# Kernel optimization log

Measured on AMD Instinct MI355X. Metric: run time of the kernel, lower is better.

## Reference

```python
import jax, jax.numpy as jnp
import numpy as np

K = 16          # num clusters
DZ = 64         # dim_zt == dim_zi (required by decoder matmul)
DT = 1024       # treatment feature dim (dim_t)
NT = 2048       # number of treatments == dim_x (columns of input_ins)
NI = 4096       # number of instances
MU_P_WT = 5.0
COS_EPS = 1e-6


def setup_inputs() -> dict:
    key = jax.random.key(0)
    ks = jax.random.split(key, 12)
    s = 0.02
    return {
        "input_ins": jax.random.uniform(ks[0], (NI, NT), dtype=jnp.float32),
        "input_treat": jax.random.normal(ks[1], (NT, DT), dtype=jnp.float32),
        # nn.Linear params (torch layout: W [out, in], y = x @ W.T + b)
        "W_mu_zt": jax.random.normal(ks[2], (DZ, DT)) * s,
        "b_mu_zt": jnp.zeros((DZ,), jnp.float32),
        "W_lv_zt": jax.random.normal(ks[3], (DZ, DT)) * s,
        "b_lv_zt": jnp.zeros((DZ,), jnp.float32),
        "W_arec": jax.random.normal(ks[4], (DT, DZ)) * s,
        "b_arec": jnp.zeros((DT,), jnp.float32),
        "W_mu_zi": jax.random.normal(ks[5], (DZ, NT)) * s,
        "b_mu_zi": jnp.zeros((DZ,), jnp.float32),
        "W_lv_zi": jax.random.normal(ks[6], (DZ, NT)) * s,
        "b_lv_zi": jnp.zeros((DZ,), jnp.float32),
        "mu_p_zt": jax.random.normal(ks[7], (K, DZ), dtype=jnp.float32),
        "logvar_p_zt": jnp.ones((K, DZ), jnp.float32),
        "W_y1": jax.random.normal(ks[8], (K * DZ, DZ)) * s,
        "b_y1": jnp.zeros((K * DZ,), jnp.float32),
        "W_y2": jax.random.normal(ks[9], (1, K * DZ)) * s,
        "b_y2": jnp.zeros((1,), jnp.float32),
    }


def reference(input_ins, input_treat, W_mu_zt, b_mu_zt, W_lv_zt, b_lv_zt,
              W_arec, b_arec, W_mu_zi, b_mu_zi, W_lv_zi, b_lv_zi,
              mu_p_zt, logvar_p_zt, W_y1, b_y1, W_y2, b_y2):
    # encode_t (eval mode: zt_sample = mu_zt)
    mu_zt = input_treat @ W_mu_zt.T + b_mu_zt           # [NT, DZ]
    logvar_zt = input_treat @ W_lv_zt.T + b_lv_zt       # [NT, DZ]
    zt = mu_zt

    # compute_qc (cosine similarity vs scaled cluster centers, *10)
    centers = MU_P_WT * mu_p_zt                          # [K, DZ]
    num = zt @ centers.T                                 # [NT, K]
    denom = jnp.maximum(
        jnp.linalg.norm(zt, axis=1, keepdims=True) * jnp.linalg.norm(centers, axis=1)[None, :],
        COS_EPS)
    qc_raw = 10.0 * num / denom                          # [NT, K]
    cates = jax.nn.softmax(qc_raw, axis=1)               # forward softmaxes qc once
    c_sample = jax.nn.softmax(cates, axis=1)             # encode_i (eval) softmaxes again

    # encode_i, vectorized over K clusters: (input_ins * cates_k) @ W.T + b
    # fused einsum avoids materializing the [K, NI, NT] masked inputs
    mu_zi = jnp.einsum('nt,tk,dt->knd', input_ins, c_sample, W_mu_zi) + b_mu_zi       # [K, NI, DZ]
    logvar_zi = jnp.einsum('nt,tk,dt->knd', input_ins, c_sample, W_lv_zi) + b_lv_zi   # [K, NI, DZ]
    zi = mu_zi  # eval-mode reparameterize

    # a_reconstby_zt
    a_reconst = jax.nn.sigmoid(zt @ W_arec.T + b_arec)   # [NT, DT]

    # decoder: sum_k sigmoid(zi_k @ zt.T) * cates_k
    logits = jnp.einsum('knd,td->knt', zi, zt)           # [K, NI, NT]
    a_pred = jnp.einsum('knt,tk->nt', jax.nn.sigmoid(logits), c_sample)  # [NI, NT]

    # predictY
    zi_all = jnp.transpose(zi, (1, 0, 2)).reshape(zi.shape[1], K * DZ)   # cat over k, dim=1
    a_zt = input_ins @ zt                                # [NI, DZ]
    rep_w1 = a_zt @ W_y1.T + b_y1                        # [NI, K*DZ]
    pred_y2 = zi_all @ W_y2.T + b_y2                     # [NI, 1]
    # diag(rep_w1 @ zi_all.T) == rowwise dot product (no NIxNI matmul)
    mu_y = jnp.sum(rep_w1 * zi_all, axis=1, keepdims=True) + pred_y2     # [NI, 1]
    logvar_y = jnp.ones_like(mu_y)

    return (mu_zt, logvar_zt, mu_p_zt, logvar_p_zt, cates, mu_zi, logvar_zi,
            zi, a_pred, mu_y, logvar_y, a_reconst)
```

## Files before the change

### kernel.cpp

```cpp
#include <hip/hip_runtime.h>

typedef unsigned short ushort_t;
typedef unsigned int   uint32;
typedef __attribute__((ext_vector_type(8))) short short8;
typedef __attribute__((ext_vector_type(4))) float f32x4;

#define DEV __device__ __forceinline__

#define KC 16
#define DZ 64
#define DT 1024
#define NT 2048
#define NI 4096
#define KD 1024

#define O_MU_ZT   0
#define O_LV_ZT   131072
#define O_MU_P    262144
#define O_LV_P    263168
#define O_CATES   264192
#define O_MU_ZI   296960
#define O_LV_ZI   4491264
#define O_ZI      8685568
#define O_APRED   12879872
#define O_MU_Y    21268480
#define O_LV_Y    21272576
#define O_AREC    21276672

#define WSF_ZT   0
#define WSF_C    131072
#define WSF_CT   163840
#define WSF_AZT  196608
#define WSF_END  458752
#define WSU_ZTB  0
#define WSU_BC   131072
#define WSU_ZIB  4325376
#define WSU_INSB 8519680
#define WSU_ZHT  16908288
#define WSU_ZLT  17039360

DEV ushort_t f2b(float f){
  uint32 u = __float_as_uint(f);
  u += 0x7fffu + ((u >> 16) & 1u);
  return (ushort_t)(u >> 16);
}
DEV uint32 pk(float lo, float hi){
  return (__float_as_uint(hi) & 0xffff0000u) | (__float_as_uint(lo) >> 16);
}
DEV float wred64(float v){
#pragma unroll
  for (int m = 32; m; m >>= 1) v += __shfl_xor(v, m, 64);
  return v;
}
DEV float fastrcp(float x){ return __builtin_amdgcn_rcpf(x); }
DEV void gl2lds16(ushort_t* l, const ushort_t* g){
  __builtin_amdgcn_global_load_lds(
      (const __attribute__((address_space(1))) unsigned int*)g,
      (__attribute__((address_space(3))) unsigned int*)l, 16, 0, 0);
}

__global__ __launch_bounds__(256) void k_encode_t(
    const float* __restrict__ treat, const float* __restrict__ Wmu,
    const float* __restrict__ bmu, const float* __restrict__ Wlv,
    const float* __restrict__ blv, float* __restrict__ out,
    float* __restrict__ ws_zt)
{
  __shared__ float rowsh[8 * DT];
  const int n0 = blockIdx.x * 8, tid = threadIdx.x;
  const float4* src = (const float4*)(treat + (size_t)n0 * DT);
#pragma unroll
  for (int i = 0; i < 8; ++i)
    ((float4*)rowsh)[tid + i * 256] = src[tid + i * 256];
  __syncthreads();
  const int j = tid & 127, half = tid >> 7;
  const bool isMu = j < 64;
  const int jj = j & 63;
  const float* W = (isMu ? Wmu : Wlv) + (size_t)jj * DT;
  const float bias = isMu ? bmu[jj] : blv[jj];
  float a0 = bias, a1 = bias, a2 = bias, a3 = bias;
  const float4* w4 = (const float4*)W;
  const float4* r0 = (const float4*)&rowsh[(half*4 + 0) * DT];
  const float4* r1 = (const float4*)&rowsh[(half*4 + 1) * DT];
  const float4* r2 = (const float4*)&rowsh[(half*4 + 2) * DT];
  const float4* r3 = (const float4*)&rowsh[(half*4 + 3) * DT];
#pragma unroll 4
  for (int i = 0; i < DT / 4; ++i){
    float4 wv = w4[i];
    float4 v0 = r0[i], v1 = r1[i], v2 = r2[i], v3 = r3[i];
    a0 += wv.x*v0.x + wv.y*v0.y + wv.z*v0.z + wv.w*v0.w;
    a1 += wv.x*v1.x + wv.y*v1.y + wv.z*v1.z + wv.w*v1.w;
    a2 += wv.x*v2.x + wv.y*v2.y + wv.z*v2.z + wv.w*v2.w;
    a3 += wv.x*v3.x + wv.y*v3.y + wv.z*v3.z + wv.w*v3.w;
  }
  float acc[4] = {a0, a1, a2, a3};
#pragma unroll
  for (int r = 0; r < 4; ++r){
    const int row = n0 + half*4 + r;
    if (isMu){ out[O_MU_ZT + row*DZ + jj] = acc[r]; ws_zt[row*DZ + jj] = acc[r]; }
    else     { out[O_LV_ZT + row*DZ + jj] = acc[r]; }
  }
}

__global__ __launch_bounds__(256) void k_qc(
    const float* __restrict__ mu_p, const float* __restrict__ ws_zt,
    float* __restrict__ out, float* __restrict__ ws_c, float* __restrict__ ws_cT)
{
  const int tid = threadIdx.x, lane = tid & 63;
  const int row = blockIdx.x * 4 + (tid >> 6);
  const float z = ws_zt[row * DZ + lane];
  const float nz = sqrtf(wred64(z * z));
  float myqc = 0.f;
#pragma unroll
  for (int k = 0; k < KC; ++k){
    float cv  = 5.f * mu_p[k * DZ + lane];
    float dot = wred64(z * cv);
    float nc2 = wred64(cv * cv);
    float qc  = 10.f * dot / fmaxf(nz * sqrtf(nc2), 1e-6f);
    if (lane == k) myqc = qc;
  }
  float mx = myqc;
#pragma unroll
  for (int m = 8; m; m >>= 1) mx = fmaxf(mx, __shfl_xor(mx, m, 16));
  float e = __expf(myqc - mx);
  float s = e;
#pragma unroll
  for (int m = 8; m; m >>= 1) s += __shfl_xor(s, m, 16);
  float cates = e / s;
  float mx2 = cates;
#pragma unroll
  for (int m = 8; m; m >>= 1) mx2 = fmaxf(mx2, __shfl_xor(mx2, m, 16));
  float e2 = __expf(cates - mx2);
  float s2 = e2;
#pragma unroll
  for (int m = 8; m; m >>= 1) s2 += __shfl_xor(s2, m, 16);
  float c2 = e2 / s2;
  if (lane < KC){
    out[O_CATES + row * KC + lane] = cates;
    ws_c[row * KC + lane] = c2;
    ws_cT[lane * NT + row] = c2;
  }
}

__global__ __launch_bounds__(256) void k_prep(
    const float* __restrict__ Wmu, const float* __restrict__ Wlv,
    const float* __restrict__ cT, const float* __restrict__ zt,
    const float* __restrict__ ins,
    ushort_t* __restrict__ Bc, ushort_t* __restrict__ ztb,
    ushort_t* __restrict__ insb,
    ushort_t* __restrict__ zhT, ushort_t* __restrict__ zlT,
    const float* __restrict__ mu_p, const float* __restrict__ lv_p,
    float* __restrict__ out)
{
  const int bx = blockIdx.x, tid = threadIdx.x;
  if (bx < 2048){
    const int j = bx;
    const bool isMu = j < KD;
    const int kk = (j & (KD-1)) >> 6, d = j & 63;
    const float* W = (isMu ? Wmu : Wlv) + (size_t)d * NT;
    const float* c = cT + (size_t)kk * NT;
    const int t = tid * 8;
    float4 w0 = *(const float4*)(W + t), w1 = *(const float4*)(W + t + 4);
    float4 c0 = *(const float4*)(c + t), c1 = *(const float4*)(c + t + 4);
    ushort_t v[8];
    v[0]=f2b(w0.x*c0.x); v[1]=f2b(w0.y*c0.y); v[2]=f2b(w0.z*c0.z); v[3]=f2b(w0.w*c0.w);
    v[4]=f2b(w1.x*c1.x); v[5]=f2b(w1.y*c1.y); v[6]=f2b(w1.z*c1.z); v[7]=f2b(w1.w*c1.w);
    *(uint4*)(Bc + (size_t)j * NT + t) = *(uint4*)v;
  } else if (bx < 2080){
    const int g = (bx - 2048) * 256 + tid;
    const int base = g * 16;
    const float4* src = (const float4*)(zt + base);
    float4 z0 = src[0], z1 = src[1], z2 = src[2], z3 = src[3];
    ushort_t v[16];
    v[0]=f2b(z0.x); v[1]=f2b(z0.y); v[2]=f2b(z0.z); v[3]=f2b(z0.w);
    v[4]=f2b(z1.x); v[5]=f2b(z1.y); v[6]=f2b(z1.z); v[7]=f2b(z1.w);
    v[8]=f2b(z2.x); v[9]=f2b(z2.y); v[10]=f2b(z2.z); v[11]=f2b(z2.w);
    v[12]=f2b(z3.x); v[13]=f2b(z3.y); v[14]=f2b(z3.z); v[15]=f2b(z3.w);
    *(uint4*)(ztb + base) = *(uint4*)&v[0];
    *(uint4*)(ztb + base + 8) = *(uint4*)&v[8];
  } else if (bx < 2084){
    const int i = (bx - 2080) * 256 + tid;
    out[O_MU_P + i] = mu_p[i];
    out[O_LV_P + i] = lv_p[i];
  } else if (bx < 4132){
    const int g = (bx - 2084) * 256 + tid;
    const int base = g * 16;
    const float4* src = (const float4*)(ins + base);
    float4 z0 = src[0], z1 = src[1], z2 = src[2], z3 = src[3];
    ushort_t v[16];
    v[0]=f2b(z0.x); v[1]=f2b(z0.y); v[2]=f2b(z0.z); v[3]=f2b(z0.w);
    v[4]=f2b(z1.x); v[5]=f2b(z1.y); v[6]=f2b(z1.z); v[7]=f2b(z1.w);
    v[8]=f2b(z2.x); v[9]=f2b(z2.y); v[10]=f2b(z2.z); v[11]=f2b(z2.w);
    v[12]=f2b(z3.x); v[13]=f2b(z3.y); v[14]=f2b(z3.z); v[15]=f2b(z3.w);
    *(uint4*)(insb + base) = *(uint4*)&v[0];
    *(uint4*)(insb + base + 8) = *(uint4*)&v[8];
  } else {
    __shared__ float zsh[64 * 65];
    const int t0 = (bx - 4132) * 64;
#pragma unroll
    for (int jj = 0; jj < 16; ++jj){
      const int idx = jj * 256 + tid;
      const int t = idx >> 6, d = idx & 63;
      zsh[t * 65 + d] = zt[(size_t)(t0 + t) * DZ + d];
    }
    __syncthreads();
    const int d = tid >> 2, tq = tid & 3;
    ushort_t vh[16], vl[16];
#pragma unroll
    for (int i = 0; i < 16; ++i){
      const float f = zsh[(tq * 16 + i) * 65 + d];
      const uint32 u = __float_as_uint(f);
      vh[i] = (ushort_t)(u >> 16);
      const float hf = __uint_as_float(u & 0xffff0000u);
      vl[i] = (ushort_t)(__float_as_uint(f - hf) >> 16);
    }
    *(uint4*)(zhT + (size_t)d * NT + t0 + tq * 16)     = *(uint4*)&vh[0];
    *(uint4*)(zhT + (size_t)d * NT + t0 + tq * 16 + 8) = *(uint4*)&vh[8];
    *(uint4*)(zlT + (size_t)d * NT + t0 + tq * 16)     = *(uint4*)&vl[0];
    *(uint4*)(zlT + (size_t)d * NT + t0 + tq * 16 + 8) = *(uint4*)&vl[8];
  }
}

__global__ __launch_bounds__(256) void k_encode_i(
    const ushort_t* __restrict__ insb, const ushort_t* __restrict__ Bc,
    const float* __restrict__ bmu, const float* __restrict__ blv,
    float* __restrict__ out, ushort_t* __restrict__ zib)
{
  __shared__ ushort_t As[128*64];
  __shared__ ushort_t Bs[128*64];
  const int tid = threadIdx.x;
  const int orig = blockIdx.y * 16 + blockIdx.x;
  const int swz  = (orig & 7) * 64 + (orig >> 3);
  const int j0 = (swz & 15) * 128, n0 = (swz >> 4) * 128;
  const int w = tid >> 6, lane = tid & 63;
  const int wm = w & 1, wn = w >> 1;
  const int l16 = lane & 15, quad = lane >> 4;

  const int srow = tid >> 3, schunk = (tid & 7) ^ (srow & 7);
  const ushort_t* aSrc = insb + (size_t)(n0 + srow) * NT + schunk * 8;
  const ushort_t* bSrc = Bc  + (size_t)(j0 + srow) * NT + schunk * 8;
  ushort_t* aDst = &As[tid * 8];
  ushort_t* bDst = &Bs[tid * 8];

  f32x4 acc[4][4] = {};

  for (int kt = 0; kt < NT/64; ++kt){
    const ushort_t* ak = aSrc + kt * 64;
    const ushort_t* bk = bSrc + kt * 64;
#pragma unroll
    for (int i = 0; i < 4; ++i){
      gl2lds16(aDst + i * 2048, ak + (size_t)i * 32 * NT);
      gl2lds16(bDst + i * 2048, bk + (size_t)i * 32 * NT);
    }
    __syncthreads();
#pragma unroll
    for (int ks = 0; ks < 2; ++ks){
      const int rsw = ((ks*4 + quad) ^ (l16 & 7)) * 8;
      short8 af[4], bf[4];
#pragma unroll
      for (int mf = 0; mf < 4; ++mf)
        af[mf] = *(const short8*)&As[(wm*64 + mf*16 + l16)*64 + rsw];
#pragma unroll
      for (int nf = 0; nf < 4; ++nf)
        bf[nf] = *(const short8*)&Bs[(wn*64 + nf*16 + l16)*64 + rsw];
#pragma unroll
      for (int mf = 0; mf < 4; ++mf)
#pragma unroll
        for (int nf = 0; nf < 4; ++nf)
          acc[mf][nf] = __builtin_amdgcn_mfma_f32_16x16x32_bf16(af[mf], bf[nf], acc[mf][nf], 0, 0, 0);
    }
    __syncthreads();
  }

  const int colW = j0 + wn * 64;
  const bool isMu = colW < KD;
  const int kk = (colW & (KD - 1)) >> 6;
  const float* bias = isMu ? bmu : blv;
  const size_t zbase = (size_t)kk * (NI * DZ);
#pragma unroll
  for (int mf = 0; mf < 4; ++mf){
    const int r = n0 + wm*64 + mf*16 + quad*4;
#pragma unroll
    for (int nf = 0; nf < 4; ++nf){
      const int d = nf*16 + l16;
      const float bv = bias[d];
#pragma unroll
      for (int reg = 0; reg < 4; ++reg){
        float v = acc[mf][nf][reg] + bv;
        size_t idx = zbase + (size_t)(r + reg)*DZ + d;
        if (isMu){
          out[O_MU_ZI + idx] = v;
          out[O_ZI + idx] = v;
          zib[idx] = f2b(v);
        } else {
          out[O_LV_ZI + idx] = v;
        }
      }
    }
  }
}

__global__ __launch_bounds__(256) void k_decoder(
    const ushort_t* __restrict__ ztb, const ushort_t* __restrict__ zib,
    const float* __restrict__ ws_c, float* __restrict__ out)
{
  __shared__ ushort_t Zt[64*64];
  __shared__ ushort_t Zi[128*64];
  __shared__ float ct[64*17];
  const int tid = threadIdx.x;
  const int t0 = blockIdx.x * 64, n0 = blockIdx.y * 128;
  const int w = tid >> 6, lane = tid & 63;
  const int wm = w & 1, wn = w >> 1;
  const int l16 = lane & 15, quad = lane >> 4;
  const int zr = tid >> 2, zq = tid & 3;
  const int ir = tid >> 1, ih = tid & 1;
  {
    const uint4* src = (const uint4*)(ztb + (size_t)(t0 + zr)*DZ + zq*16);
    uint4 z0 = src[0], z1 = src[1];
    ushort_t* dst = &Zt[zr*64];
    *(uint4*)&dst[((zq*2 + 0) ^ (zr & 7)) * 8] = z0;
    *(uint4*)&dst[((zq*2 + 1) ^ (zr & 7)) * 8] = z1;
  }
  for (int i = tid; i < 64*16; i += 256){
    int t = i >> 4, k = i & 15;
    ct[t*17 + k] = ws_c[(size_t)(t0 + t)*KC + k];
  }
  __syncthreads();
  short8 bfh[2][2];
#pragma unroll
  for (int ks = 0; ks < 2; ++ks){
    const int rsw = ((ks*4 + quad) ^ (l16 & 7)) * 8;
#pragma unroll
    for (int nf = 0; nf < 2; ++nf)
      bfh[ks][nf] = *(const short8*)&Zt[(wn*32 + nf*16 + l16)*64 + rsw];
  }
  const ushort_t* iG = zib + (size_t)(n0 + ir)*DZ + ih*32;
  ushort_t* isw = &Zi[ir*64];
  const int sw0 = ((ih*4 + 0) ^ (ir & 7)) * 8;
  const int sw1 = ((ih*4 + 1) ^ (ir & 7)) * 8;
  const int sw2 = ((ih*4 + 2) ^ (ir & 7)) * 8;
  const int sw3 = ((ih*4 + 3) ^ (ir & 7)) * 8;
  uint4 Zr0, Zr1, Zr2, Zr3;
  {
    const uint4* zp = (const uint4*)iG;
    Zr0 = zp[0]; Zr1 = zp[1]; Zr2 = zp[2]; Zr3 = zp[3];
  }
  f32x4 accum[4][2] = {};
  for (int k = 0; k < KC; ++k){
    __syncthreads();
    *(uint4*)&isw[sw0] = Zr0; *(uint4*)&isw[sw1] = Zr1;
    *(uint4*)&isw[sw2] = Zr2; *(uint4*)&isw[sw3] = Zr3;
    __syncthreads();
    if (k < KC - 1){
      const uint4* zp = (const uint4*)(iG + (size_t)(k+1)*(NI*DZ));
      Zr0 = zp[0]; Zr1 = zp[1]; Zr2 = zp[2]; Zr3 = zp[3];
    }
    f32x4 s[4][2] = {};
#pragma unroll
    for (int ks = 0; ks < 2; ++ks){
      const int rsw = ((ks*4 + quad) ^ (l16 & 7)) * 8;
      short8 af[4];
#pragma unroll
      for (int mf = 0; mf < 4; ++mf)
        af[mf] = *(const short8*)&Zi[(wm*64 + mf*16 + l16)*64 + rsw];
#pragma unroll
      for (int mf = 0; mf < 4; ++mf)
#pragma unroll
        for (int nf = 0; nf < 2; ++nf)
          s[mf][nf] = __builtin_amdgcn_mfma_f32_16x16x32_bf16(af[mf], bfh[ks][nf], s[mf][nf], 0, 0, 0);
    }
#pragma unroll
    for (int nf = 0; nf < 2; ++nf){
      const float cv = ct[(wn*32 + nf*16 + l16)*17 + k];
#pragma unroll
      for (int mf = 0; mf < 4; ++mf)
#pragma unroll
        for (int reg = 0; reg < 4; ++reg)
          accum[mf][nf][reg] += cv * fastrcp(1.f + __expf(-s[mf][nf][reg]));
    }
  }
#pragma unroll
  for (int mf = 0; mf < 4; ++mf){
    const int r = n0 + wm*64 + mf*16 + quad*4;
#pragma unroll
    for (int nf = 0; nf < 2; ++nf){
      const int col = t0 + wn*32 + nf*16 + l16;
#pragma unroll
      for (int reg = 0; reg < 4; ++reg)
        out[O_APRED + (size_t)(r + reg)*NT + col] = accum[mf][nf][reg];
    }
  }
}

__global__ __launch_bounds__(512) void k_arec(
    const float* __restrict__ ws_zt, const float* __restrict__ W,
    const float* __restrict__ bias, float* __restrict__ out)
{
  __shared__ float zsh[8 * DZ];
  const int n0 = blockIdx.x * 8, tid = threadIdx.x;
  if (tid < 128)
    ((float4*)zsh)[tid] = ((const float4*)(ws_zt + (size_t)n0 * DZ))[tid];
  __syncthreads();
#pragma unroll
  for (int jo = 0; jo < 2; ++jo){
    const int j = jo*512 + tid;
    const float4* w4 = (const float4*)(W + (size_t)j * DZ);
    const float b = bias[j];
    float acc[8];
#pragma unroll
    for (int r = 0; r < 8; ++r) acc[r] = b;
#pragma unroll
    for (int i = 0; i < 16; ++i){
      float4 wv = w4[i];
#pragma unroll
      for (int r = 0; r < 8; ++r){
        const float* z = &zsh[r*DZ + i*4];
        acc[r] += wv.x*z[0] + wv.y*z[1] + wv.z*z[2] + wv.w*z[3];
      }
    }
#pragma unroll
    for (int r = 0; r < 8; ++r)
      out[O_AREC + (size_t)(n0 + r)*DT + j] = fastrcp(1.f + __expf(-acc[r]));
  }
}

__global__ __launch_bounds__(512) void k_azt(
    const float* __restrict__ ins, const ushort_t* __restrict__ zhT,
    const ushort_t* __restrict__ zlT, float* __restrict__ azt)
{
  __shared__ float red[16*64];
  const int tid = threadIdx.x;
  const int n0 = blockIdx.x * 16;
  const int w = tid >> 6, lane = tid & 63;
  const int kh = w >> 2, wd = w & 3;
  const int l16 = lane & 15, quad = lane >> 4;
  const float* aRow = ins + (size_t)(n0 + l16) * NT + kh * 1024 + quad * 8;
  const ushort_t* bh = zhT + (size_t)(wd * 16 + l16) * NT + kh * 1024 + quad * 8;
  const ushort_t* bl = zlT + (size_t)(wd * 16 + l16) * NT + kh * 1024 + quad * 8;
  f32x4 acc = {};
#pragma unroll 4
  for (int kt = 0; kt < 16; ++kt){
#pragma unroll
    for (int ks = 0; ks < 2; ++ks){
      const int ko = kt * 64 + ks * 32;
      float4 a0 = *(const float4*)(aRow + ko);
      float4 a1 = *(const float4*)(aRow + ko + 4);
      uint32 u0 = __float_as_uint(a0.x), u1 = __float_as_uint(a0.y);
      uint32 u2 = __float_as_uint(a0.z), u3 = __float_as_uint(a0.w);
      uint32 u4 = __float_as_uint(a1.x), u5 = __float_as_uint(a1.y);
      uint32 u6 = __float_as_uint(a1.z), u7 = __float_as_uint(a1.w);
      uint4 H, L;
      H.x = (u1 & 0xffff0000u) | (u0 >> 16);
      H.y = (u3 & 0xffff0000u) | (u2 >> 16);
      H.z = (u5 & 0xffff0000u) | (u4 >> 16);
      H.w = (u7 & 0xffff0000u) | (u6 >> 16);
      float l0 = a0.x - __uint_as_float(u0 & 0xffff0000u);
      float l1 = a0.y - __uint_as_float(u1 & 0xffff0000u);
      float l2 = a0.z - __uint_as_float(u2 & 0xffff0000u);
      float l3 = a0.w - __uint_as_float(u3 & 0xffff0000u);
      float l4 = a1.x - __uint_as_float(u4 & 0xffff0000u);
      float l5 = a1.y - __uint_as_float(u5 & 0xffff0000u);
      float l6 = a1.z - __uint_as_float(u6 & 0xffff0000u);
      float l7 = a1.w - __uint_as_float(u7 & 0xffff0000u);
      L.x = pk(l0, l1); L.y = pk(l2, l3); L.z = pk(l4, l5); L.w = pk(l6, l7);
      short8 ah = *(short8*)&H, al = *(short8*)&L;
      short8 bh8 = *(const short8*)(bh + ko);
      short8 bl8 = *(const short8*)(bl + ko);
      acc = __builtin_amdgcn_mfma_f32_16x16x32_bf16(ah, bh8, acc, 0, 0, 0);
      acc = __builtin_amdgcn_mfma_f32_16x16x32_bf16(al, bh8, acc, 0, 0, 0);
      acc = __builtin_amdgcn_mfma_f32_16x16x32_bf16(ah, bl8, acc, 0, 0, 0);
    }
  }
  const int col = wd * 16 + l16;
  if (kh == 1){
#pragma unroll
    for (int reg = 0; reg < 4; ++reg)
      red[(quad*4 + reg)*64 + col] = acc[reg];
  }
  __syncthreads();
  if (kh == 0){
#pragma unroll
    for (int reg = 0; reg < 4; ++reg)
      azt[(size_t)(n0 + quad*4 + reg) * DZ + col] = acc[reg] + red[(quad*4 + reg)*64 + col];
  }
}

__global__ __launch_bounds__(512) void k_muy(
    const float* __restrict__ azt, const float* __restrict__ Wy1,
    const float* __restrict__ by1, const float* __restrict__ Wy2,
    const float* __restrict__ by2, const float* __restrict__ zi_out,
    float* __restrict__ out)
{
  __shared__ float sazt[16][DZ];
  const int tid = threadIdx.x;
  const int n0 = blockIdx.x * 16;
  for (int i = tid; i < 16*DZ; i += 512)
    sazt[i >> 6][i & 63] = azt[(size_t)(n0 + (i >> 6))*DZ + (i & 63)];
  __syncthreads();
  const int w = tid >> 6, lane = tid & 63;
  float s0 = 0.f, s1 = 0.f;
  for (int jj = 0; jj < 16; ++jj){
    const int j = jj*64 + lane;
    const float4* wr = (const float4*)(Wy1 + (size_t)j * DZ);
    float d0 = 0.f, d1 = 0.f;
    const float* a0 = sazt[w*2 + 0];
    const float* a1 = sazt[w*2 + 1];
#pragma unroll
    for (int i = 0; i < 16; ++i){
      float4 wv = wr[i];
      d0 += wv.x*a0[i*4] + wv.y*a0[i*4+1] + wv.z*a0[i*4+2] + wv.w*a0[i*4+3];
      d1 += wv.x*a1[i*4] + wv.y*a1[i*4+1] + wv.z*a1[i*4+2] + wv.w*a1[i*4+3];
    }
    const float add = by1[j] + Wy2[j];
    const size_t zb = (size_t)jj*(NI*DZ) + lane;
    s0 += (d0 + add) * zi_out[zb + (size_t)(n0 + w*2 + 0)*DZ];
    s1 += (d1 + add) * zi_out[zb + (size_t)(n0 + w*2 + 1)*DZ];
  }
  s0 = wred64(s0); s1 = wred64(s1);
  if (lane == 0){
    const float b = by2[0];
    out[O_MU_Y + n0 + w*2 + 0] = s0 + b;
    out[O_MU_Y + n0 + w*2 + 1] = s1 + b;
  }
  if (tid < 16) out[O_LV_Y + n0 + tid] = 1.0f;
}

extern "C" void kernel_launch(void* const* d_in, const int* in_sizes, int n_in,
                              void* d_out, int out_size, void* d_ws, size_t ws_size,
                              hipStream_t stream)
{
  (void)in_sizes; (void)n_in; (void)out_size; (void)ws_size;
  const float* ins   = (const float*)d_in[0];
  const float* treat = (const float*)d_in[1];
  const float* Wmzt  = (const float*)d_in[2];
  const float* bmzt  = (const float*)d_in[3];
  const float* Wlzt  = (const float*)d_in[4];
  const float* blzt  = (const float*)d_in[5];
  const float* Warec = (const float*)d_in[6];
  const float* barec = (const float*)d_in[7];
  const float* Wmzi  = (const float*)d_in[8];
  const float* bmzi  = (const float*)d_in[9];
  const float* Wlzi  = (const float*)d_in[10];
  const float* blzi  = (const float*)d_in[11];
  const float* mu_p  = (const float*)d_in[12];
  const float* lv_p  = (const float*)d_in[13];
  const float* Wy1   = (const float*)d_in[14];
  const float* by1   = (const float*)d_in[15];
  const float* Wy2   = (const float*)d_in[16];
  const float* by2   = (const float*)d_in[17];
  float* out = (float*)d_out;
  float* wsf = (float*)d_ws;
  ushort_t* wsu = (ushort_t*)(wsf + WSF_END);

  float* ws_zt  = wsf + WSF_ZT;
  float* ws_c   = wsf + WSF_C;
  float* ws_cT  = wsf + WSF_CT;
  float* ws_azt = wsf + WSF_AZT;
  ushort_t* ztb  = wsu + WSU_ZTB;
  ushort_t* Bc   = wsu + WSU_BC;
  ushort_t* zib  = wsu + WSU_ZIB;
  ushort_t* insb = wsu + WSU_INSB;
  ushort_t* zhT  = wsu + WSU_ZHT;
  ushort_t* zlT  = wsu + WSU_ZLT;

  k_encode_t<<<NT/8, 256, 0, stream>>>(treat, Wmzt, bmzt, Wlzt, blzt, out, ws_zt);
  k_qc      <<<NT/4, 256, 0, stream>>>(mu_p, ws_zt, out, ws_c, ws_cT);
  k_prep    <<<4164, 256, 0, stream>>>(Wmzi, Wlzi, ws_cT, ws_zt, ins, Bc, ztb, insb, zhT, zlT, mu_p, lv_p, out);
  k_encode_i<<<dim3(16, 32), 256, 0, stream>>>(insb, Bc, bmzi, blzi, out, zib);
  k_decoder <<<dim3(32, 32), 256, 0, stream>>>(ztb, zib, ws_c, out);
  k_arec    <<<NT/8, 512, 0, stream>>>(ws_zt, Warec, barec, out);
  k_azt     <<<NI/16, 512, 0, stream>>>(ins, zhT, zlT, ws_azt);
  k_muy     <<<NI/16, 512, 0, stream>>>(ws_azt, Wy1, by1, Wy2, by2, out + O_ZI, out);
}
```

Measured before the change: 426.5 us.

## Transpose W_y1 in prep and restructure k_muy for coalesced reuse

Adds a k_prep branch that transposes W_y1 into a [DZ, K*DZ] workspace buffer. k_muy is rewritten so each thread owns two output columns j and accumulates all 16 rows of a block. Each W_y1 element is then loaded once per block with coalesced reads, where before each thread read a strided 256-byte row per row pair. The cost is extra prep blocks, 32 accumulators per thread, and a shared-memory cross-wave reduction.

```diff
diff --git a/kernel.cpp b/kernel.cpp
--- a/kernel.cpp
+++ b/kernel.cpp
@@ -38,6 +38,7 @@
 #define WSU_INSB 8519680
 #define WSU_ZHT  16908288
 #define WSU_ZLT  17039360
+#define WSU_END  17170432
 
 DEV ushort_t f2b(float f){
   uint32 u = __float_as_uint(f);
@@ -144,10 +145,11 @@
 __global__ __launch_bounds__(256) void k_prep(
     const float* __restrict__ Wmu, const float* __restrict__ Wlv,
     const float* __restrict__ cT, const float* __restrict__ zt,
-    const float* __restrict__ ins,
+    const float* __restrict__ ins, const float* __restrict__ Wy1,
     ushort_t* __restrict__ Bc, ushort_t* __restrict__ ztb,
     ushort_t* __restrict__ insb,
     ushort_t* __restrict__ zhT, ushort_t* __restrict__ zlT,
+    float* __restrict__ w1T,
     const float* __restrict__ mu_p, const float* __restrict__ lv_p,
     float* __restrict__ out)
 {
@@ -193,7 +195,7 @@
     v[12]=f2b(z3.x); v[13]=f2b(z3.y); v[14]=f2b(z3.z); v[15]=f2b(z3.w);
     *(uint4*)(insb + base) = *(uint4*)&v[0];
     *(uint4*)(insb + base + 8) = *(uint4*)&v[8];
-  } else {
+  } else if (bx < 4164){
     __shared__ float zsh[64 * 65];
     const int t0 = (bx - 4132) * 64;
 #pragma unroll
@@ -217,6 +219,25 @@
     *(uint4*)(zhT + (size_t)d * NT + t0 + tq * 16 + 8) = *(uint4*)&vh[8];
     *(uint4*)(zlT + (size_t)d * NT + t0 + tq * 16)     = *(uint4*)&vl[0];
     *(uint4*)(zlT + (size_t)d * NT + t0 + tq * 16 + 8) = *(uint4*)&vl[8];
+  } else {
+    __shared__ float wsh[64 * 65];
+    const int j0 = (bx - 4164) * 64;
+#pragma unroll
+    for (int jj = 0; jj < 16; ++jj){
+      const int idx = jj * 256 + tid;
+      const int r = idx >> 6, d = idx & 63;
+      wsh[r * 65 + d] = Wy1[(size_t)(j0 + r) * DZ + d];
+    }
+    __syncthreads();
+    const int d = tid >> 2, q = tid & 3;
+    float v[16];
+#pragma unroll
+    for (int i = 0; i < 16; ++i) v[i] = wsh[(q*16 + i)*65 + d];
+#pragma unroll
+    for (int i = 0; i < 4; ++i){
+      float4 o; o.x = v[i*4]; o.y = v[i*4+1]; o.z = v[i*4+2]; o.w = v[i*4+3];
+      *(float4*)&w1T[(size_t)d * KD + j0 + q*16 + i*4] = o;
+    }
   }
 }
 
@@ -485,43 +506,55 @@
 }
 
 __global__ __launch_bounds__(512) void k_muy(
-    const float* __restrict__ azt, const float* __restrict__ Wy1,
+    const float* __restrict__ azt, const float* __restrict__ w1T,
     const float* __restrict__ by1, const float* __restrict__ Wy2,
     const float* __restrict__ by2, const float* __restrict__ zi_out,
     float* __restrict__ out)
 {
   __shared__ float sazt[16][DZ];
+  __shared__ float sred[8][16];
   const int tid = threadIdx.x;
   const int n0 = blockIdx.x * 16;
   for (int i = tid; i < 16*DZ; i += 512)
     sazt[i >> 6][i & 63] = azt[(size_t)(n0 + (i >> 6))*DZ + (i & 63)];
   __syncthreads();
   const int w = tid >> 6, lane = tid & 63;
-  float s0 = 0.f, s1 = 0.f;
-  for (int jj = 0; jj < 16; ++jj){
-    const int j = jj*64 + lane;
-    const float4* wr = (const float4*)(Wy1 + (size_t)j * DZ);
-    float d0 = 0.f, d1 = 0.f;
-    const float* a0 = sazt[w*2 + 0];
-    const float* a1 = sazt[w*2 + 1];
-#pragma unroll
-    for (int i = 0; i < 16; ++i){
-      float4 wv = wr[i];
-      d0 += wv.x*a0[i*4] + wv.y*a0[i*4+1] + wv.z*a0[i*4+2] + wv.w*a0[i*4+3];
-      d1 += wv.x*a1[i*4] + wv.y*a1[i*4+1] + wv.z*a1[i*4+2] + wv.w*a1[i*4+3];
-    }
-    const float add = by1[j] + Wy2[j];
-    const size_t zb = (size_t)jj*(NI*DZ) + lane;
-    s0 += (d0 + add) * zi_out[zb + (size_t)(n0 + w*2 + 0)*DZ];
-    s1 += (d1 + add) * zi_out[zb + (size_t)(n0 + w*2 + 1)*DZ];
-  }
-  s0 = wred64(s0); s1 = wred64(s1);
-  if (lane == 0){
-    const float b = by2[0];
-    out[O_MU_Y + n0 + w*2 + 0] = s0 + b;
-    out[O_MU_Y + n0 + w*2 + 1] = s1 + b;
-  }
-  if (tid < 16) out[O_LV_Y + n0 + tid] = 1.0f;
+  const int jA = w*128 + lane, jB = jA + 64;
+  float repA[16] = {}, repB[16] = {};
+#pragma unroll 4
+  for (int d4 = 0; d4 < 16; ++d4){
+    const float* wrow = w1T + (size_t)(d4*4) * KD;
+    const float wa0 = wrow[jA],        wb0 = wrow[jB];
+    const float wa1 = wrow[KD + jA],   wb1 = wrow[KD + jB];
+    const float wa2 = wrow[2*KD + jA], wb2 = wrow[2*KD + jB];
+    const float wa3 = wrow[3*KD + jA], wb3 = wrow[3*KD + jB];
+#pragma unroll
+    for (int n = 0; n < 16; ++n){
+      float4 av = *(const float4*)&sazt[n][d4*4];
+      repA[n] += av.x*wa0 + av.y*wa1 + av.z*wa2 + av.w*wa3;
+      repB[n] += av.x*wb0 + av.y*wb1 + av.z*wb2 + av.w*wb3;
+    }
+  }
+  const float addA = by1[jA] + Wy2[jA];
+  const float addB = by1[jB] + Wy2[jB];
+  const size_t zbA = (size_t)(w*2    ) * (NI*DZ) + lane;
+  const size_t zbB = (size_t)(w*2 + 1) * (NI*DZ) + lane;
+#pragma unroll
+  for (int n = 0; n < 16; ++n){
+    const size_t ro = (size_t)(n0 + n) * DZ;
+    float p = (repA[n] + addA) * zi_out[zbA + ro]
+            + (repB[n] + addB) * zi_out[zbB + ro];
+    p = wred64(p);
+    if (lane == 0) sred[w][n] = p;
+  }
+  __syncthreads();
+  if (tid < 16){
+    float s = by2[0];
+#pragma unroll
+    for (int ww = 0; ww < 8; ++ww) s += sred[ww][tid];
+    out[O_MU_Y + n0 + tid] = s;
+    out[O_LV_Y + n0 + tid] = 1.0f;
+  }
 }
 
 extern "C" void kernel_launch(void* const* d_in, const int* in_sizes, int n_in,
@@ -561,13 +594,14 @@
   ushort_t* insb = wsu + WSU_INSB;
   ushort_t* zhT  = wsu + WSU_ZHT;
   ushort_t* zlT  = wsu + WSU_ZLT;
+  float* w1T     = (float*)(wsu + WSU_END);
 
   k_encode_t<<<NT/8, 256, 0, stream>>>(treat, Wmzt, bmzt, Wlzt, blzt, out, ws_zt);
   k_qc      <<<NT/4, 256, 0, stream>>>(mu_p, ws_zt, out, ws_c, ws_cT);
-  k_prep    <<<4164, 256, 0, stream>>>(Wmzi, Wlzi, ws_cT, ws_zt, ins, Bc, ztb, insb, zhT, zlT, mu_p, lv_p, out);
+  k_prep    <<<4180, 256, 0, stream>>>(Wmzi, Wlzi, ws_cT, ws_zt, ins, Wy1, Bc, ztb, insb, zhT, zlT, w1T, mu_p, lv_p, out);
   k_encode_i<<<dim3(16, 32), 256, 0, stream>>>(insb, Bc, bmzi, blzi, out, zib);
   k_decoder <<<dim3(32, 32), 256, 0, stream>>>(ztb, zib, ws_c, out);
   k_arec    <<<NT/8, 512, 0, stream>>>(ws_zt, Warec, barec, out);
   k_azt     <<<NI/16, 512, 0, stream>>>(ins, zhT, zlT, ws_azt);
-  k_muy     <<<NI/16, 512, 0, stream>>>(ws_azt, Wy1, by1, Wy2, by2, out + O_ZI, out);
-}
+  k_muy     <<<NI/16, 512, 0, stream>>>(ws_azt, w1T, by1, Wy2, by2, out + O_ZI, out);
+}
```

Result: faster. 401.2 us (-5.9%).
